# Kernel tuning notes

Hardware: AMD Instinct MI355X
Metric: run time of the kernel (lower is better)

Reference implementation:

```python
import jax, jax.numpy as jnp
import numpy as np

B, N, D_IN = 128, 128, 1024
H1, D_OUT = 256, 32
K = 8  # num_clusters


def setup_inputs() -> dict:
    key = jax.random.key(0)
    ks = jax.random.split(key, 3)
    x = jax.random.normal(ks[0], (B, N, D_IN), dtype=jnp.float32)
    W1 = jax.random.normal(ks[1], (D_IN, H1), dtype=jnp.float32) * (1.0 / np.sqrt(D_IN))
    b1 = jnp.zeros((H1,), jnp.float32)
    W2 = jax.random.normal(ks[2], (H1, D_OUT), dtype=jnp.float32) * (1.0 / np.sqrt(H1))
    b2 = jnp.zeros((D_OUT,), jnp.float32)
    return {"x": x, "W1": W1, "b1": b1, "W2": W2, "b2": b2}


def _mlp(x, W1, b1, W2, b2):
    # nn.Sequential(GELU, Linear(1024,256), GELU, Linear(256,32)); torch GELU default = exact erf
    h = jax.nn.gelu(x, approximate=False)
    h = h @ W1 + b1
    h = jax.nn.gelu(h, approximate=False)
    return h @ W2 + b2  # [B, N, 32]


def _ward_labels(feats, k):
    """Greedy ward-linkage agglomerative clustering of feats [n, d] -> int labels [n].
    Ward merge cost d(A,B) = |A||B|/(|A|+|B|) * ||c_A - c_B||^2 (Lance-Williams equiv)."""
    n = feats.shape[0]
    eye = jnp.eye(n, dtype=bool)

    def body(t, state):
        cents, sizes, lab = state
        sq = jnp.sum(cents * cents, axis=-1)
        d2 = jnp.maximum(sq[:, None] + sq[None, :] - 2.0 * (cents @ cents.T), 0.0)
        w = (sizes[:, None] * sizes[None, :]) / (sizes[:, None] + sizes[None, :] + 1e-30)
        active = sizes > 0
        valid = (active[:, None] & active[None, :]) & (~eye)
        Dm = jnp.where(valid, w * d2, jnp.inf)
        idx = jnp.argmin(Dm)
        i, j = idx // n, idx % n
        i2 = jnp.minimum(i, j)
        j2 = jnp.maximum(i, j)
        si, sj = sizes[i2], sizes[j2]
        newc = (cents[i2] * si + cents[j2] * sj) / (si + sj)
        cents = cents.at[i2].set(newc)
        sizes = sizes.at[i2].set(si + sj).at[j2].set(0.0)
        lab = jnp.where(lab == j2, i2, lab)
        return cents, sizes, lab

    init = (feats, jnp.ones((n,), feats.dtype), jnp.arange(n))
    cents, sizes, lab = jax.lax.fori_loop(0, n - k, body, init)
    # relabel surviving representative indices to 0..k-1 (ordered by index)
    rank = jnp.cumsum((sizes > 0).astype(jnp.int32)) - 1
    return rank[lab]


def reference(x, W1, b1, W2, b2):
    feats = _mlp(x, W1, b1, W2, b2)          # [B, N, 32]
    labels = jax.vmap(lambda f: _ward_labels(f, K))(feats)  # [B, N] int32
    return labels
```

## Files before the change

### kernel.cpp

```cpp
#include <hip/hip_runtime.h>
#include <math.h>

#define BB 128
#define NN 128
#define DIN 1024
#define H1 256
#define DOUT 32
#define KCL 8
#define NPTS 128
#define MROWS (BB*NN)
#define CSTR 130
#define RSTR 132
#define DEADKEY 0xFFFFFFFF00000000ull

__device__ __forceinline__ float gelu_exact(float v) {
    return 0.5f * v * (1.0f + erff(v * 0.70710678118654752f));
}

__device__ __forceinline__ unsigned long long mkkey(float v, int r, int j) {
    return ((unsigned long long)__float_as_uint(v) << 32) | (unsigned)((r << 7) | j);
}

__device__ __forceinline__ float readlanef(float v, int lane) {
    return __int_as_float(__builtin_amdgcn_readlane(__float_as_int(v), lane));
}

template<int CTRL, int RMASK>
__device__ __forceinline__ unsigned dpp_umin_step(unsigned v) {
    unsigned t = (unsigned)__builtin_amdgcn_update_dpp((int)v, (int)v, CTRL, RMASK, 0xf, false);
    return t < v ? t : v;
}
__device__ __forceinline__ unsigned wave_umin_bcast(unsigned v) {
    v = dpp_umin_step<0x111, 0xf>(v);
    v = dpp_umin_step<0x112, 0xf>(v);
    v = dpp_umin_step<0x114, 0xf>(v);
    v = dpp_umin_step<0x118, 0xf>(v);
    v = dpp_umin_step<0x142, 0xa>(v);
    v = dpp_umin_step<0x143, 0xc>(v);
    return (unsigned)__builtin_amdgcn_readlane((int)v, 63);
}
__device__ __forceinline__ unsigned half_umin(unsigned v) {
    v = dpp_umin_step<0x111, 0xf>(v);
    v = dpp_umin_step<0x112, 0xf>(v);
    v = dpp_umin_step<0x114, 0xf>(v);
    v = dpp_umin_step<0x118, 0xf>(v);
    v = dpp_umin_step<0x142, 0xa>(v);
    return v;
}

__global__ __launch_bounds__(256) void gelu_kernel(const float* __restrict__ x,
                                                   float* __restrict__ gx, int n4) {
    int i = blockIdx.x * 256 + threadIdx.x;
    const int stride = gridDim.x * 256;
    for (; i < n4; i += stride) {
        float4 v = ((const float4*)x)[i];
        v.x = gelu_exact(v.x);
        v.y = gelu_exact(v.y);
        v.z = gelu_exact(v.z);
        v.w = gelu_exact(v.w);
        ((float4*)gx)[i] = v;
    }
}

template<bool FUSE>
__global__ __launch_bounds__(256) void mlp1_kernel(const float* __restrict__ xin,
                                                   const float* __restrict__ W1,
                                                   const float* __restrict__ b1,
                                                   float* __restrict__ h) {
    __shared__ float As[32][68];
    __shared__ float Bs[32][68];
    const int bm = blockIdx.x;
    const int bn = blockIdx.y;
    const int tid = threadIdx.x;
    const int tx = tid & 15, ty = tid >> 4;

    float acc[4][4] = {{0.f}};

    const int arow = tid >> 2;
    const int acol4 = (tid & 3) * 4;
    const int brow = tid >> 4;
    const int bcol4 = (tid & 15) * 4;

    const float* xrow = xin + (size_t)(bm * 64 + arow) * DIN;
    const float* wbase = W1 + bn * 64;

    for (int kt = 0; kt < DIN; kt += 32) {
        float4 a0 = *(const float4*)(xrow + kt + acol4);
        float4 a1 = *(const float4*)(xrow + kt + 16 + acol4);
        float4 w0 = *(const float4*)(wbase + (size_t)(kt + brow) * H1 + bcol4);
        float4 w1 = *(const float4*)(wbase + (size_t)(kt + 16 + brow) * H1 + bcol4);
        __syncthreads();
        if (FUSE) {
            As[acol4 + 0][arow] = gelu_exact(a0.x);
            As[acol4 + 1][arow] = gelu_exact(a0.y);
            As[acol4 + 2][arow] = gelu_exact(a0.z);
            As[acol4 + 3][arow] = gelu_exact(a0.w);
            As[16 + acol4 + 0][arow] = gelu_exact(a1.x);
            As[16 + acol4 + 1][arow] = gelu_exact(a1.y);
            As[16 + acol4 + 2][arow] = gelu_exact(a1.z);
            As[16 + acol4 + 3][arow] = gelu_exact(a1.w);
        } else {
            As[acol4 + 0][arow] = a0.x;
            As[acol4 + 1][arow] = a0.y;
            As[acol4 + 2][arow] = a0.z;
            As[acol4 + 3][arow] = a0.w;
            As[16 + acol4 + 0][arow] = a1.x;
            As[16 + acol4 + 1][arow] = a1.y;
            As[16 + acol4 + 2][arow] = a1.z;
            As[16 + acol4 + 3][arow] = a1.w;
        }
        *(float4*)&Bs[brow][bcol4] = w0;
        *(float4*)&Bs[16 + brow][bcol4] = w1;
        __syncthreads();
#pragma unroll
        for (int kk = 0; kk < 32; ++kk) {
            float4 a = *(const float4*)&As[kk][ty * 4];
            float4 b = *(const float4*)&Bs[kk][tx * 4];
            float ar[4] = {a.x, a.y, a.z, a.w};
            float br[4] = {b.x, b.y, b.z, b.w};
#pragma unroll
            for (int i = 0; i < 4; ++i)
#pragma unroll
                for (int j = 0; j < 4; ++j)
                    acc[i][j] = fmaf(ar[i], br[j], acc[i][j]);
        }
    }

    const int row = bm * 64 + ty * 4;
    const int col = bn * 64 + tx * 4;
    float4 bias = *(const float4*)(b1 + col);
#pragma unroll
    for (int i = 0; i < 4; ++i) {
        float4 o;
        o.x = acc[i][0] + bias.x;
        o.y = acc[i][1] + bias.y;
        o.z = acc[i][2] + bias.z;
        o.w = acc[i][3] + bias.w;
        *(float4*)(h + (size_t)(row + i) * H1 + col) = o;
    }
}

__global__ __launch_bounds__(256) void mlp2_kernel(const float* __restrict__ h,
                                                   const float* __restrict__ W2,
                                                   const float* __restrict__ b2,
                                                   float* __restrict__ feats) {
    __shared__ float hs[16][257];
    __shared__ float w2s[H1 * DOUT];
    const int blk = blockIdx.x;
    const int tid = threadIdx.x;

    for (int i = tid; i < (H1 * DOUT) / 4; i += 256) {
        ((float4*)w2s)[i] = ((const float4*)W2)[i];
    }
    const float* hb = h + (size_t)blk * 16 * H1;
    for (int i = tid; i < (16 * H1) / 4; i += 256) {
        float4 v = ((const float4*)hb)[i];
        int r = i >> 6;
        int c = (i & 63) * 4;
        hs[r][c + 0] = gelu_exact(v.x);
        hs[r][c + 1] = gelu_exact(v.y);
        hs[r][c + 2] = gelu_exact(v.z);
        hs[r][c + 3] = gelu_exact(v.w);
    }
    __syncthreads();

    const int col = tid & 31;
    const int r0 = (tid >> 5) * 2;
    float acc0 = 0.f, acc1 = 0.f;
    for (int k = 0; k < H1; ++k) {
        float w = w2s[k * DOUT + col];
        acc0 = fmaf(hs[r0 + 0][k], w, acc0);
        acc1 = fmaf(hs[r0 + 1][k], w, acc1);
    }
    float bias = b2[col];
    const int rowg = blk * 16 + r0;
    feats[(size_t)(rowg + 0) * DOUT + col] = acc0 + bias;
    feats[(size_t)(rowg + 1) * DOUT + col] = acc1 + bias;
}

__global__ __launch_bounds__(256) void ward_kernel(const float* __restrict__ feats,
                                                   int* __restrict__ out) {
    __shared__ __align__(16) float cost[NPTS * RSTR];
    __shared__ __align__(16) float G[NPTS * RSTR];
    __shared__ float centsT[32 * CSTR];
    __shared__ unsigned long long rowkey[NPTS];
    __shared__ float sqArr[NPTS];
    __shared__ float szsE[NPTS];
    __shared__ int rnk[NPTS];

    const int b = blockIdx.x;
    const int tid = threadIdx.x;
    const float* f = feats + (size_t)b * NPTS * DOUT;
    const float INF = __builtin_inff();

    for (int i = tid; i < NPTS * DOUT; i += 256) {
        int r = i >> 5, d = i & 31;
        centsT[d * CSTR + r] = f[i];
    }
    __syncthreads();
    if (tid < NPTS) {
        float s = 0.f;
#pragma unroll
        for (int d = 0; d < 32; ++d) {
            float v = centsT[d * CSTR + tid];
            s = fmaf(v, v, s);
        }
        sqArr[tid] = s;
    }
    __syncthreads();
    {
        int ti = tid >> 4, tj = tid & 15;
        int I0 = ti * 8, J0 = tj * 8;
        float acc[8][8];
#pragma unroll
        for (int u = 0; u < 8; ++u)
#pragma unroll
            for (int v = 0; v < 8; ++v) acc[u][v] = 0.f;
        for (int d = 0; d < 32; ++d) {
            float a[8], bb[8];
#pragma unroll
            for (int u = 0; u < 8; ++u) a[u] = centsT[d * CSTR + I0 + u];
#pragma unroll
            for (int v = 0; v < 8; ++v) bb[v] = centsT[d * CSTR + J0 + v];
#pragma unroll
            for (int u = 0; u < 8; ++u)
#pragma unroll
                for (int v = 0; v < 8; ++v)
                    acc[u][v] = fmaf(a[u], bb[v], acc[u][v]);
        }
#pragma unroll
        for (int u = 0; u < 8; ++u) {
#pragma unroll
            for (int v = 0; v < 8; ++v) {
                int i = I0 + u, j = J0 + v;
                G[i * RSTR + j] = acc[u][v];
                float d2 = sqArr[i] + sqArr[j] - 2.0f * acc[u][v];
                if (d2 < 0.f) d2 = 0.f;
                float w = (1.0f * 1.0f) / (1.0f + 1.0f + 1e-30f);
                cost[i * RSTR + j] = (i == j) ? INF : w * d2;
            }
        }
    }
    __syncthreads();
    if (tid < NPTS) {
        unsigned long long best = DEADKEY;
        for (int j = 0; j < NPTS; ++j) {
            float v = cost[tid * RSTR + j];
            unsigned long long k = mkkey(v, tid, j);
            if (k < best) best = k;
        }
        rowkey[tid] = best;
    }
    __syncthreads();

    if (tid >= 64) return;
    const int lane = tid;
    const int hh = lane & 31;
    const int r0 = lane * 2, r1 = lane * 2 + 1;

    unsigned long long k0 = rowkey[r0], k1 = rowkey[r1];
    float q0 = sqArr[r0], q1 = sqArr[r1];
    float s0 = 1.0f, s1 = 1.0f;
    int lab0 = r0, lab1 = r1;
    unsigned long long alive0 = ~0ull, alive1 = ~0ull;

    for (int it = 0; it < NPTS - KCL; ++it) {
        unsigned bv0 = (unsigned)(k0 >> 32), bv1 = (unsigned)(k1 >> 32);
        unsigned lmin = bv0 < bv1 ? bv0 : bv1;
        unsigned lflat = (bv0 <= bv1) ? (unsigned)(k0 & 0x3FFFu) : (unsigned)(k1 & 0x3FFFu);
        unsigned gmin = wave_umin_bcast(lmin);
        unsigned long long bmask = __ballot(lmin == gmin);
        int lsel = __ffsll(bmask) - 1;
        unsigned flat = (unsigned)__builtin_amdgcn_readlane((int)lflat, lsel);
        int ra = (int)(flat >> 7), ca = (int)(flat & 127u);
        const int i2 = ra < ca ? ra : ca;
        const int j2 = ra < ca ? ca : ra;

        float2 gi = *(const float2*)&G[i2 * RSTR + r0];
        float2 gj = *(const float2*)&G[j2 * RSTR + r0];

        float si = readlanef((i2 & 1) ? s1 : s0, i2 >> 1);
        float sj = readlanef((j2 & 1) ? s1 : s0, j2 >> 1);
        const float snew = si + sj;
        const float invs = 1.0f / snew;
        const float wa = si * invs, wb = sj * invs;

        int arg0 = (int)(k0 & 127u), arg1 = (int)(k1 & 127u);
        bool d0 = (s0 > 0.f) && r0 != i2 && r0 != j2 && (arg0 == i2 || arg0 == j2);
        bool d1 = (s1 > 0.f) && r1 != i2 && r1 != j2 && (arg1 == i2 || arg1 == j2);
        unsigned long long m0 = __ballot(d0), m1 = __ballot(d1);

        float Gii = readlanef((i2 & 1) ? gi.y : gi.x, i2 >> 1);
        float Gij = readlanef((i2 & 1) ? gj.y : gj.x, i2 >> 1);
        float Gjj = readlanef((j2 & 1) ? gj.y : gj.x, j2 >> 1);
        float dotA = wa * Gii + wb * Gij;
        float dotB = wa * Gij + wb * Gjj;
        float qn = wa * dotA + wb * dotB;

        float dot0 = wa * gi.x + wb * gj.x;
        float dot1 = wa * gi.y + wb * gj.y;

        if (lab0 == j2) lab0 = i2;
        if (lab1 == j2) lab1 = i2;
        if (r0 == i2) s0 = snew; else if (r0 == j2) { s0 = 0.f; k0 = DEADKEY; }
        if (r1 == i2) s1 = snew; else if (r1 == j2) { s1 = 0.f; k1 = DEADKEY; }
        if (j2 < 64) alive0 &= ~(1ull << j2); else alive1 &= ~(1ull << (j2 - 64));
        if (r0 == i2) { dot0 = qn; q0 = qn; }
        if (r1 == i2) { dot1 = qn; q1 = qn; }

        *(float2*)&G[i2 * RSTR + r0] = make_float2(dot0, dot1);
        G[r0 * RSTR + i2] = dot0;
        G[r1 * RSTR + i2] = dot1;

        bool w0 = (s0 > 0.f) && r0 != i2 && r0 != j2;
        bool w1 = (s1 > 0.f) && r1 != i2 && r1 != j2;
        if (w0) {
            float d2 = q0 + qn - 2.0f * dot0;
            if (d2 < 0.f) d2 = 0.f;
            float w = (s0 * snew) / (s0 + snew + 1e-30f);
            float v0 = w * d2;
            cost[r0 * RSTR + i2] = v0;
            cost[i2 * RSTR + r0] = v0;
            if (!d0) {
                unsigned long long nk = mkkey(v0, r0, i2);
                if (nk < k0) k0 = nk;
            }
        }
        if (w1) {
            float d2 = q1 + qn - 2.0f * dot1;
            if (d2 < 0.f) d2 = 0.f;
            float w = (s1 * snew) / (s1 + snew + 1e-30f);
            float v1 = w * d2;
            cost[r1 * RSTR + i2] = v1;
            cost[i2 * RSTR + r1] = v1;
            if (!d1) {
                unsigned long long nk = mkkey(v1, r1, i2);
                if (nk < k1) k1 = nk;
            }
        }

        bool pi = true;
        unsigned long long mm0 = m0, mm1 = m1;
        while (pi | (mm0 != 0ull) | (mm1 != 0ull)) {
            int rA, rB;
            bool hasB = false;
            if (pi) { rA = i2; pi = false; }
            else if (mm0) { int t = __ffsll(mm0) - 1; rA = 2 * t; mm0 &= mm0 - 1; }
            else { int t = __ffsll(mm1) - 1; rA = 2 * t + 1; mm1 &= mm1 - 1; }
            if (mm0) { int t = __ffsll(mm0) - 1; rB = 2 * t; mm0 &= mm0 - 1; hasB = true; }
            else if (mm1) { int t = __ffsll(mm1) - 1; rB = 2 * t + 1; mm1 &= mm1 - 1; hasB = true; }
            else rB = rA;

            int r = (lane < 32) ? rA : rB;
            float4 cv = *(const float4*)&cost[r * RSTR + 4 * hh];
            unsigned long long word = (hh < 16) ? alive0 : alive1;
            unsigned nib = (unsigned)(word >> ((4 * hh) & 63)) & 0xFu;
            unsigned e0 = (nib & 1u) ? __float_as_uint(cv.x) : 0xFFFFFFFFu;
            unsigned e1 = (nib & 2u) ? __float_as_uint(cv.y) : 0xFFFFFFFFu;
            unsigned e2 = (nib & 4u) ? __float_as_uint(cv.z) : 0xFFFFFFFFu;
            unsigned e3 = (nib & 8u) ? __float_as_uint(cv.w) : 0xFFFFFFFFu;
            unsigned m = e0; int c = 0;
            if (e1 < m) { m = e1; c = 1; }
            if (e2 < m) { m = e2; c = 2; }
            if (e3 < m) { m = e3; c = 3; }
            int lcol = 4 * hh + c;
            unsigned hm = half_umin(m);
            unsigned vA = (unsigned)__builtin_amdgcn_readlane((int)hm, 31);
            unsigned vB = (unsigned)__builtin_amdgcn_readlane((int)hm, 63);
            unsigned vref = (lane < 32) ? vA : vB;
            unsigned long long msk = __ballot(m == vref);
            int laneA = __ffsll(msk & 0xFFFFFFFFull) - 1;
            int laneB = 32 + __ffsll(msk >> 32) - 1;
            int colA = __builtin_amdgcn_readlane(lcol, laneA);
            int colB = __builtin_amdgcn_readlane(lcol, laneB);
            unsigned long long keyA = ((unsigned long long)vA << 32) | (unsigned)((rA << 7) | colA);
            unsigned long long keyB = ((unsigned long long)vB << 32) | (unsigned)((rB << 7) | colB);
            if (lane == (rA >> 1)) { if (rA & 1) k1 = keyA; else k0 = keyA; }
            if (hasB && lane == (rB >> 1)) { if (rB & 1) k1 = keyB; else k0 = keyB; }
        }
    }

    szsE[r0] = s0;
    szsE[r1] = s1;
    __asm__ volatile("s_waitcnt lgkmcnt(0)" ::: "memory");
    if (lane == 0) {
        int c = 0;
        for (int i = 0; i < NPTS; ++i) rnk[i] = (szsE[i] > 0.f) ? c++ : -1;
    }
    __asm__ volatile("s_waitcnt lgkmcnt(0)" ::: "memory");
    out[b * NPTS + r0] = rnk[lab0];
    out[b * NPTS + r1] = rnk[lab1];
}

extern "C" void kernel_launch(void* const* d_in, const int* in_sizes, int n_in,
                              void* d_out, int out_size, void* d_ws, size_t ws_size,
                              hipStream_t stream) {
    const float* x  = (const float*)d_in[0];
    const float* W1 = (const float*)d_in[1];
    const float* b1 = (const float*)d_in[2];
    const float* W2 = (const float*)d_in[3];
    const float* b2 = (const float*)d_in[4];

    float* h = (float*)d_ws;
    float* feats = h + (size_t)MROWS * H1;
    float* gx = feats + (size_t)MROWS * DOUT;
    int* out = (int*)d_out;

    const size_t need = ((size_t)MROWS * H1 + (size_t)MROWS * DOUT + (size_t)MROWS * DIN) * 4;
    const bool use_gx = ws_size >= need;

    if (use_gx) {
        gelu_kernel<<<2048, 256, 0, stream>>>(x, gx, MROWS * DIN / 4);
        mlp1_kernel<false><<<dim3(MROWS / 64, H1 / 64), 256, 0, stream>>>(gx, W1, b1, h);
    } else {
        mlp1_kernel<true><<<dim3(MROWS / 64, H1 / 64), 256, 0, stream>>>(x, W1, b1, h);
    }
    mlp2_kernel<<<MROWS / 16, 256, 0, stream>>>(h, W2, b2, feats);
    ward_kernel<<<BB, 256, 0, stream>>>(feats, out);
}
```

Measured before the change: 428.9 us.

## Enlarge mlp1 GEMM tile to 128x64 with double-buffered shared memory

```diff
diff --git a/kernel.cpp b/kernel.cpp
--- a/kernel.cpp
+++ b/kernel.cpp
@@ -67,76 +67,113 @@
                                                    const float* __restrict__ W1,
                                                    const float* __restrict__ b1,
                                                    float* __restrict__ h) {
-    __shared__ float As[32][68];
-    __shared__ float Bs[32][68];
+    __shared__ float As[2][16][132];
+    __shared__ float Bs[2][16][68];
     const int bm = blockIdx.x;
     const int bn = blockIdx.y;
     const int tid = threadIdx.x;
-    const int tx = tid & 15, ty = tid >> 4;
-
-    float acc[4][4] = {{0.f}};
-
-    const int arow = tid >> 2;
-    const int acol4 = (tid & 3) * 4;
-    const int brow = tid >> 4;
-    const int bcol4 = (tid & 15) * 4;
-
-    const float* xrow = xin + (size_t)(bm * 64 + arow) * DIN;
+    const int tx = tid & 15;
+    const int ty = tid >> 4;
+
+    float acc[8][4];
+#pragma unroll
+    for (int i = 0; i < 8; ++i)
+#pragma unroll
+        for (int j = 0; j < 4; ++j) acc[i][j] = 0.f;
+
+    const int arow = tid >> 1;
+    const int ak8  = (tid & 1) * 8;
+    const int bk   = tid >> 4;
+    const int bcol = (tid & 15) * 4;
+
+    const float* xrow = xin + (size_t)(bm * 128 + arow) * DIN;
     const float* wbase = W1 + bn * 64;
 
-    for (int kt = 0; kt < DIN; kt += 32) {
-        float4 a0 = *(const float4*)(xrow + kt + acol4);
-        float4 a1 = *(const float4*)(xrow + kt + 16 + acol4);
-        float4 w0 = *(const float4*)(wbase + (size_t)(kt + brow) * H1 + bcol4);
-        float4 w1 = *(const float4*)(wbase + (size_t)(kt + 16 + brow) * H1 + bcol4);
-        __syncthreads();
-        if (FUSE) {
-            As[acol4 + 0][arow] = gelu_exact(a0.x);
-            As[acol4 + 1][arow] = gelu_exact(a0.y);
-            As[acol4 + 2][arow] = gelu_exact(a0.z);
-            As[acol4 + 3][arow] = gelu_exact(a0.w);
-            As[16 + acol4 + 0][arow] = gelu_exact(a1.x);
-            As[16 + acol4 + 1][arow] = gelu_exact(a1.y);
-            As[16 + acol4 + 2][arow] = gelu_exact(a1.z);
-            As[16 + acol4 + 3][arow] = gelu_exact(a1.w);
-        } else {
-            As[acol4 + 0][arow] = a0.x;
-            As[acol4 + 1][arow] = a0.y;
-            As[acol4 + 2][arow] = a0.z;
-            As[acol4 + 3][arow] = a0.w;
-            As[16 + acol4 + 0][arow] = a1.x;
-            As[16 + acol4 + 1][arow] = a1.y;
-            As[16 + acol4 + 2][arow] = a1.z;
-            As[16 + acol4 + 3][arow] = a1.w;
-        }
-        *(float4*)&Bs[brow][bcol4] = w0;
-        *(float4*)&Bs[16 + brow][bcol4] = w1;
-        __syncthreads();
-#pragma unroll
-        for (int kk = 0; kk < 32; ++kk) {
-            float4 a = *(const float4*)&As[kk][ty * 4];
-            float4 b = *(const float4*)&Bs[kk][tx * 4];
-            float ar[4] = {a.x, a.y, a.z, a.w};
-            float br[4] = {b.x, b.y, b.z, b.w};
-#pragma unroll
-            for (int i = 0; i < 4; ++i)
+    float4 a0 = *(const float4*)(xrow + ak8);
+    float4 a1 = *(const float4*)(xrow + ak8 + 4);
+    float4 w0 = *(const float4*)(wbase + (size_t)bk * H1 + bcol);
+    if (FUSE) {
+        As[0][ak8 + 0][arow] = gelu_exact(a0.x);
+        As[0][ak8 + 1][arow] = gelu_exact(a0.y);
+        As[0][ak8 + 2][arow] = gelu_exact(a0.z);
+        As[0][ak8 + 3][arow] = gelu_exact(a0.w);
+        As[0][ak8 + 4][arow] = gelu_exact(a1.x);
+        As[0][ak8 + 5][arow] = gelu_exact(a1.y);
+        As[0][ak8 + 6][arow] = gelu_exact(a1.z);
+        As[0][ak8 + 7][arow] = gelu_exact(a1.w);
+    } else {
+        As[0][ak8 + 0][arow] = a0.x;
+        As[0][ak8 + 1][arow] = a0.y;
+        As[0][ak8 + 2][arow] = a0.z;
+        As[0][ak8 + 3][arow] = a0.w;
+        As[0][ak8 + 4][arow] = a1.x;
+        As[0][ak8 + 5][arow] = a1.y;
+        As[0][ak8 + 6][arow] = a1.z;
+        As[0][ak8 + 7][arow] = a1.w;
+    }
+    *(float4*)&Bs[0][bk][bcol] = w0;
+    __syncthreads();
+
+    int cur = 0;
+    for (int kt = 0; kt < DIN; kt += 16) {
+        const bool has_next = (kt + 16) < DIN;
+        if (has_next) {
+            a0 = *(const float4*)(xrow + kt + 16 + ak8);
+            a1 = *(const float4*)(xrow + kt + 16 + ak8 + 4);
+            w0 = *(const float4*)(wbase + (size_t)(kt + 16 + bk) * H1 + bcol);
+        }
+#pragma unroll
+        for (int kk = 0; kk < 16; ++kk) {
+            float4 aL = *(const float4*)&As[cur][kk][ty * 4];
+            float4 aH = *(const float4*)&As[cur][kk][64 + ty * 4];
+            float4 bv = *(const float4*)&Bs[cur][kk][tx * 4];
+            float ar[8] = {aL.x, aL.y, aL.z, aL.w, aH.x, aH.y, aH.z, aH.w};
+            float br[4] = {bv.x, bv.y, bv.z, bv.w};
+#pragma unroll
+            for (int i = 0; i < 8; ++i)
 #pragma unroll
                 for (int j = 0; j < 4; ++j)
                     acc[i][j] = fmaf(ar[i], br[j], acc[i][j]);
         }
-    }
-
-    const int row = bm * 64 + ty * 4;
-    const int col = bn * 64 + tx * 4;
-    float4 bias = *(const float4*)(b1 + col);
-#pragma unroll
-    for (int i = 0; i < 4; ++i) {
+        if (has_next) {
+            const int nxt = cur ^ 1;
+            if (FUSE) {
+                As[nxt][ak8 + 0][arow] = gelu_exact(a0.x);
+                As[nxt][ak8 + 1][arow] = gelu_exact(a0.y);
+                As[nxt][ak8 + 2][arow] = gelu_exact(a0.z);
+                As[nxt][ak8 + 3][arow] = gelu_exact(a0.w);
+                As[nxt][ak8 + 4][arow] = gelu_exact(a1.x);
+                As[nxt][ak8 + 5][arow] = gelu_exact(a1.y);
+                As[nxt][ak8 + 6][arow] = gelu_exact(a1.z);
+                As[nxt][ak8 + 7][arow] = gelu_exact(a1.w);
+            } else {
+                As[nxt][ak8 + 0][arow] = a0.x;
+                As[nxt][ak8 + 1][arow] = a0.y;
+                As[nxt][ak8 + 2][arow] = a0.z;
+                As[nxt][ak8 + 3][arow] = a0.w;
+                As[nxt][ak8 + 4][arow] = a1.x;
+                As[nxt][ak8 + 5][arow] = a1.y;
+                As[nxt][ak8 + 6][arow] = a1.z;
+                As[nxt][ak8 + 7][arow] = a1.w;
+            }
+            *(float4*)&Bs[nxt][bk][bcol] = w0;
+        }
+        __syncthreads();
+        cur ^= 1;
+    }
+
+    const int row0 = bm * 128 + ty * 4;
+    const int col0 = bn * 64 + tx * 4;
+    float4 bias = *(const float4*)(b1 + col0);
+#pragma unroll
+    for (int i = 0; i < 8; ++i) {
+        const int rr = (i < 4) ? i : (64 + i - 4);
         float4 o;
         o.x = acc[i][0] + bias.x;
         o.y = acc[i][1] + bias.y;
         o.z = acc[i][2] + bias.z;
         o.w = acc[i][3] + bias.w;
-        *(float4*)(h + (size_t)(row + i) * H1 + col) = o;
+        *(float4*)(h + (size_t)(row0 + rr) * H1 + col0) = o;
     }
 }
 
@@ -411,9 +448,9 @@
 
     if (use_gx) {
         gelu_kernel<<<2048, 256, 0, stream>>>(x, gx, MROWS * DIN / 4);
-        mlp1_kernel<false><<<dim3(MROWS / 64, H1 / 64), 256, 0, stream>>>(gx, W1, b1, h);
+        mlp1_kernel<false><<<dim3(MROWS / 128, H1 / 64), 256, 0, stream>>>(gx, W1, b1, h);
     } else {
-        mlp1_kernel<true><<<dim3(MROWS / 64, H1 / 64), 256, 0, stream>>>(x, W1, b1, h);
+        mlp1_kernel<true><<<dim3(MROWS / 128, H1 / 64), 256, 0, stream>>>(x, W1, b1, h);
     }
     mlp2_kernel<<<MROWS / 16, 256, 0, stream>>>(h, W2, b2, feats);
     ward_kernel<<<BB, 256, 0, stream>>>(feats, out);
```

New measurement: 489.2 us. 14.1% more time.

## Fuse second MLP layer into ward clustering kernel

Applied to the files above, without the earlier changes.

```diff
diff --git a/kernel.cpp b/kernel.cpp
--- a/kernel.cpp
+++ b/kernel.cpp
@@ -11,6 +11,7 @@
 #define MROWS (BB*NN)
 #define CSTR 130
 #define RSTR 132
+#define HSTR 257
 #define DEADKEY 0xFFFFFFFF00000000ull
 
 __device__ __forceinline__ float gelu_exact(float v) {
@@ -140,45 +141,9 @@
     }
 }
 
-__global__ __launch_bounds__(256) void mlp2_kernel(const float* __restrict__ h,
+__global__ __launch_bounds__(256) void ward_kernel(const float* __restrict__ h,
                                                    const float* __restrict__ W2,
                                                    const float* __restrict__ b2,
-                                                   float* __restrict__ feats) {
-    __shared__ float hs[16][257];
-    __shared__ float w2s[H1 * DOUT];
-    const int blk = blockIdx.x;
-    const int tid = threadIdx.x;
-
-    for (int i = tid; i < (H1 * DOUT) / 4; i += 256) {
-        ((float4*)w2s)[i] = ((const float4*)W2)[i];
-    }
-    const float* hb = h + (size_t)blk * 16 * H1;
-    for (int i = tid; i < (16 * H1) / 4; i += 256) {
-        float4 v = ((const float4*)hb)[i];
-        int r = i >> 6;
-        int c = (i & 63) * 4;
-        hs[r][c + 0] = gelu_exact(v.x);
-        hs[r][c + 1] = gelu_exact(v.y);
-        hs[r][c + 2] = gelu_exact(v.z);
-        hs[r][c + 3] = gelu_exact(v.w);
-    }
-    __syncthreads();
-
-    const int col = tid & 31;
-    const int r0 = (tid >> 5) * 2;
-    float acc0 = 0.f, acc1 = 0.f;
-    for (int k = 0; k < H1; ++k) {
-        float w = w2s[k * DOUT + col];
-        acc0 = fmaf(hs[r0 + 0][k], w, acc0);
-        acc1 = fmaf(hs[r0 + 1][k], w, acc1);
-    }
-    float bias = b2[col];
-    const int rowg = blk * 16 + r0;
-    feats[(size_t)(rowg + 0) * DOUT + col] = acc0 + bias;
-    feats[(size_t)(rowg + 1) * DOUT + col] = acc1 + bias;
-}
-
-__global__ __launch_bounds__(256) void ward_kernel(const float* __restrict__ feats,
                                                    int* __restrict__ out) {
     __shared__ __align__(16) float cost[NPTS * RSTR];
     __shared__ __align__(16) float G[NPTS * RSTR];
@@ -190,14 +155,52 @@
 
     const int b = blockIdx.x;
     const int tid = threadIdx.x;
-    const float* f = feats + (size_t)b * NPTS * DOUT;
     const float INF = __builtin_inff();
 
-    for (int i = tid; i < NPTS * DOUT; i += 256) {
-        int r = i >> 5, d = i & 31;
-        centsT[d * CSTR + r] = f[i];
+    {
+        float* w2s = G;
+        float* hs = cost;
+        for (int i = tid; i < (H1 * DOUT) / 4; i += 256)
+            ((float4*)w2s)[i] = ((const float4*)W2)[i];
+        const float4 bias = ((const float4*)b2)[tid & 7];
+        const float* hb = h + (size_t)b * NPTS * H1;
+
+        const int sr = tid & 31;
+        const int sk = (tid >> 5) * 32;
+        const int row = tid >> 3;
+        const int col4 = (tid & 7) * 4;
+
+        for (int c = 0; c < 4; ++c) {
+            __syncthreads();
+            const float* hrow = hb + (size_t)(c * 32 + sr) * H1 + sk;
+#pragma unroll
+            for (int j = 0; j < 8; ++j) {
+                float4 v = ((const float4*)hrow)[j];
+                hs[sr * HSTR + sk + 4 * j + 0] = gelu_exact(v.x);
+                hs[sr * HSTR + sk + 4 * j + 1] = gelu_exact(v.y);
+                hs[sr * HSTR + sk + 4 * j + 2] = gelu_exact(v.z);
+                hs[sr * HSTR + sk + 4 * j + 3] = gelu_exact(v.w);
+            }
+            __syncthreads();
+            float a0 = 0.f, a1 = 0.f, a2 = 0.f, a3 = 0.f;
+            const float* hr = &hs[row * HSTR];
+            for (int k = 0; k < H1; ++k) {
+                float a = hr[k];
+                float4 w = *(const float4*)&w2s[k * DOUT + col4];
+                a0 = fmaf(a, w.x, a0);
+                a1 = fmaf(a, w.y, a1);
+                a2 = fmaf(a, w.z, a2);
+                a3 = fmaf(a, w.w, a3);
+            }
+            const int gr = c * 32 + row;
+            centsT[(col4 + 0) * CSTR + gr] = a0 + bias.x;
+            centsT[(col4 + 1) * CSTR + gr] = a1 + bias.y;
+            centsT[(col4 + 2) * CSTR + gr] = a2 + bias.z;
+            centsT[(col4 + 3) * CSTR + gr] = a3 + bias.w;
+        }
     }
     __syncthreads();
+
     if (tid < NPTS) {
         float s = 0.f;
 #pragma unroll
@@ -402,11 +405,10 @@
     const float* b2 = (const float*)d_in[4];
 
     float* h = (float*)d_ws;
-    float* feats = h + (size_t)MROWS * H1;
-    float* gx = feats + (size_t)MROWS * DOUT;
+    float* gx = h + (size_t)MROWS * H1;
     int* out = (int*)d_out;
 
-    const size_t need = ((size_t)MROWS * H1 + (size_t)MROWS * DOUT + (size_t)MROWS * DIN) * 4;
+    const size_t need = ((size_t)MROWS * H1 + (size_t)MROWS * DIN) * 4;
     const bool use_gx = ws_size >= need;
 
     if (use_gx) {
@@ -415,6 +417,5 @@
     } else {
         mlp1_kernel<true><<<dim3(MROWS / 64, H1 / 64), 256, 0, stream>>>(x, W1, b1, h);
     }
-    mlp2_kernel<<<MROWS / 16, 256, 0, stream>>>(h, W2, b2, feats);
-    ward_kernel<<<BB, 256, 0, stream>>>(feats, out);
-}
+    ward_kernel<<<BB, 256, 0, stream>>>(h, W2, b2, out);
+}
```

After: 441.7 us. +3.0%, slower.
